# Kernel optimization log

Measured on AMD Instinct MI355X. Metric: run time of the kernel, lower is better.

Reference implementation:

```python
import jax, jax.numpy as jnp
import numpy as np

BETA = 1.0  # config.beta
B, G, K, E2 = 1024, 512, 128, 128


def setup_inputs() -> dict:
    key = jax.random.key(0)
    k1, k2, k3, k4, k5 = jax.random.split(key, 5)
    s = 0.05
    return {
        "images": jax.random.normal(k1, (B, G), dtype=jnp.float32),
        "wimg": jax.random.normal(k2, (G, K), dtype=jnp.float32) * s,    # project.weight.T
        "wrec": jax.random.normal(k3, (K, E2), dtype=jnp.float32) * s,   # rec.weight.T
        "wrec2": jax.random.normal(k4, (K + 1, E2), dtype=jnp.float32) * s,  # rec2.weight.T
        "wimg2": jax.random.normal(k5, (G, K, K + 1), dtype=jnp.float32) * s,  # img2.weight.T.reshape(K+1,K,G).T
    }


def _soft_assign(x, codes):
    # x: [B, D], codes: [D, C] -> softmax over C of -beta * mean_D (x - codes)^2
    xh = -jnp.mean((x[:, :, None] - codes[None]) ** 2, axis=1) * BETA  # [B, C]
    return jax.nn.softmax(xh, axis=-1)


def reference(images, wimg, wrec, wrec2, wimg2):
    # ---- encode ----
    xp = _soft_assign(images, wimg)            # [B, K]
    lat = xp @ wrec                            # [B, E2]
    xp = _soft_assign(lat, wrec.T)             # [B, K] (codes are wrec.T: [E2, K])
    idx = jnp.argmax(xp, axis=-1)              # [B] hard component
    xwimg = jnp.transpose(wimg2[:, idx, :], (1, 0, 2))   # [B, G, K+1]
    base = wimg[:, idx].T[:, :, None]                     # [B, G, 1]
    xd = images[:, :, None] - base - xwimg                # [B, G, K+1]
    xh2 = -jnp.mean(xd ** 2, axis=1) * BETA               # [B, K+1]
    xp2 = jax.nn.softmax(xh2, axis=-1)
    lat2 = xp2 @ wrec2                                    # [B, E2]
    # ---- decode (ret='rec', n_step>=1) ----
    xp_d = _soft_assign(lat, wrec.T)           # [B, K]
    xp2_d = _soft_assign(lat2, wrec2.T)        # [B, K+1]
    wimgg = wimg[:, :, None] + wimg2           # [G, K, K+1]
    # tensordot(xp_d[:, :, None]*xp2_d[:, None, :], wimgg.permute(1,2,0), 2)
    xrec = jnp.einsum('bk,bj,gkj->bg', xp_d, xp2_d, wimgg)  # [B, G]
    # ---- loss ----
    loss = jnp.mean((xrec - images) ** 2, axis=-1)  # [B]
    return loss
```

## Files before the change

### kernel.cpp

```cpp
#include <hip/hip_runtime.h>

#define B_    1024
#define G_    512
#define K_    128
#define J_    129
#define JP_   130
#define E2_   128
#define KK_   16512
#define KK2_  16640
#define KKE2_ 16768
#define KKP_  16896
#define SPLITS 16
#define KCHUNK 1056
#define BK_   32
#define KSTEPS 33
#define GS_   8

using short8 = __attribute__((ext_vector_type(8))) short;
using f32x4  = __attribute__((ext_vector_type(4))) float;

__device__ __forceinline__ float bf2f(unsigned short h){
  return __uint_as_float(((unsigned int)h) << 16);
}
__device__ __forceinline__ unsigned short f2bf(float f){
  unsigned int u = __float_as_uint(f);
  u += 0x7fffu + ((u >> 16) & 1u);
  return (unsigned short)(u >> 16);
}

__device__ __forceinline__ float blockSum512(float v, float* red, int t){
  #pragma unroll
  for (int off = 32; off > 0; off >>= 1) v += __shfl_down(v, off);
  __syncthreads();
  if ((t & 63) == 0) red[t >> 6] = v;
  __syncthreads();
  float r = ((red[0] + red[1]) + (red[2] + red[3]))
          + ((red[4] + red[5]) + (red[6] + red[7]));
  __syncthreads();
  return r;
}
__device__ __forceinline__ float blockMax512(float v, float* red, int t){
  #pragma unroll
  for (int off = 32; off > 0; off >>= 1) v = fmaxf(v, __shfl_down(v, off));
  __syncthreads();
  if ((t & 63) == 0) red[t >> 6] = v;
  __syncthreads();
  float r = fmaxf(fmaxf(fmaxf(red[0], red[1]), fmaxf(red[2], red[3])),
                  fmaxf(fmaxf(red[4], red[5]), fmaxf(red[6], red[7])));
  __syncthreads();
  return r;
}
__device__ __forceinline__ int blockArgmax512(float v, int i, float* redf, int* redi, int t){
  #pragma unroll
  for (int off = 32; off > 0; off >>= 1){
    float ov = __shfl_down(v, off);
    int   oi = __shfl_down(i, off);
    if (ov > v || (ov == v && oi < i)){ v = ov; i = oi; }
  }
  __syncthreads();
  if ((t & 63) == 0){ redf[t >> 6] = v; redi[t >> 6] = i; }
  __syncthreads();
  float bv = redf[0]; int bi = redi[0];
  #pragma unroll
  for (int wv = 1; wv < 8; wv++){
    float ov = redf[wv]; int oi = redi[wv];
    if (ov > bv || (ov == bv && oi < bi)){ bv = ov; bi = oi; }
  }
  __syncthreads();
  return bi;
}

__global__ __launch_bounds__(1024) void norms_kernel(
    const float* __restrict__ wimg, const float* __restrict__ wrec,
    const float* __restrict__ wrec2, float* __restrict__ c1norm,
    float* __restrict__ w3norm, float* __restrict__ w6norm,
    float* __restrict__ wrecT, float* __restrict__ wrec2T){
  int t = threadIdx.x;
  if (blockIdx.x == 0){
    __shared__ float red[8][128];
    int k = t & 127, sl = t >> 7;
    float s = 0.f;
    int g0 = sl * (G_/8);
    for (int g = g0; g < g0 + G_/8; g++){
      float v = wimg[g*K_ + k]; s += v*v;
    }
    red[sl][k] = s;
    __syncthreads();
    if (t < 128){
      float r = 0.f;
      #pragma unroll
      for (int i = 0; i < 8; i++) r += red[i][t];
      c1norm[t] = r;
    }
  } else if (blockIdx.x == 1){
    int wave = t >> 6, lane = t & 63;
    for (int k = wave; k < K_; k += 16){
      float v0 = wrec[k*E2_ + lane], v1 = wrec[k*E2_ + 64 + lane];
      float s = v0*v0 + v1*v1;
      #pragma unroll
      for (int off = 32; off > 0; off >>= 1) s += __shfl_down(s, off);
      if (lane == 0) w3norm[k] = s;
    }
  } else if (blockIdx.x == 2){
    int wave = t >> 6, lane = t & 63;
    for (int j = wave; j < J_; j += 16){
      float v0 = wrec2[j*E2_ + lane], v1 = wrec2[j*E2_ + 64 + lane];
      float s = v0*v0 + v1*v1;
      #pragma unroll
      for (int off = 32; off > 0; off >>= 1) s += __shfl_down(s, off);
      if (lane == 0) w6norm[j] = s;
    }
  } else if (blockIdx.x == 3){
    for (int n = t; n < K_*E2_; n += 1024){
      int k = n >> 7, e = n & 127;
      wrecT[e*K_ + k] = wrec[n];
    }
  } else {
    for (int n = t; n < J_*E2_; n += 1024){
      int j = n >> 7, e = n & 127;
      wrec2T[e*J_ + j] = wrec2[n];
    }
  }
}

__global__ __launch_bounds__(128) void tables_part_kernel(
    const float* __restrict__ wimg2, const float* __restrict__ wimg,
    float* __restrict__ sqp, float* __restrict__ crp,
    unsigned short* __restrict__ W2){
  int n  = blockIdx.x * 128 + threadIdx.x;
  int gs = blockIdx.y;
  int k = n / J_;
  int w2i = n + k;
  float s0=0,s1=0,s2=0,s3=0, c0=0,c1=0,c2=0,c3=0;
  int gbase = gs * (G_/GS_);
  #pragma unroll 2
  for (int g = gbase; g < gbase + G_/GS_; g += 4){
    float w0 = wimg2[(size_t)(g  )*KK_ + n];
    float w1 = wimg2[(size_t)(g+1)*KK_ + n];
    float w2 = wimg2[(size_t)(g+2)*KK_ + n];
    float w3 = wimg2[(size_t)(g+3)*KK_ + n];
    W2[(size_t)(g  )*KKP_ + w2i] = f2bf(w0);
    W2[(size_t)(g+1)*KKP_ + w2i] = f2bf(w1);
    W2[(size_t)(g+2)*KKP_ + w2i] = f2bf(w2);
    W2[(size_t)(g+3)*KKP_ + w2i] = f2bf(w3);
    s0 += w0*w0; s1 += w1*w1; s2 += w2*w2; s3 += w3*w3;
    c0 += wimg[(g  )*K_ + k]*w0;
    c1 += wimg[(g+1)*K_ + k]*w1;
    c2 += wimg[(g+2)*K_ + k]*w2;
    c3 += wimg[(g+3)*K_ + k]*w3;
  }
  sqp[(size_t)gs*KK_ + n] = (s0+s1)+(s2+s3);
  crp[(size_t)gs*KK_ + n] = (c0+c1)+(c2+c3);
}
__global__ __launch_bounds__(128) void tables_reduce_kernel(
    const float* __restrict__ sqp, const float* __restrict__ crp,
    float* __restrict__ sq2, float* __restrict__ cross){
  int n = blockIdx.x * 128 + threadIdx.x;
  float s = 0.f, c = 0.f;
  #pragma unroll
  for (int gs = 0; gs < GS_; gs++){
    s += sqp[(size_t)gs*KK_ + n];
    c += crp[(size_t)gs*KK_ + n];
  }
  sq2[n] = s; cross[n] = c;
}

__global__ __launch_bounds__(128) void w2tail_kernel(
    const float* __restrict__ wimg, unsigned short* __restrict__ W2){
  int g = blockIdx.x, t = threadIdx.x;
  unsigned short* dst = W2 + (size_t)g * KKP_;
  dst[KK2_ + t]   = f2bf(wimg[g*K_ + t]);
  dst[KKE2_ + t]  = 0;
  dst[t*JP_ + 129] = 0;
}

__global__ __launch_bounds__(512, 8) void encdec_kernel(
    const float* __restrict__ img,  const float* __restrict__ wimg,
    const float* __restrict__ wrec, const float* __restrict__ wrec2,
    const float* __restrict__ wrecT, const float* __restrict__ wrec2T,
    const unsigned short* __restrict__ W2,
    const float* __restrict__ c1norm, const float* __restrict__ w3norm,
    const float* __restrict__ w6norm, const float* __restrict__ sq2,
    const float* __restrict__ cross, unsigned short* __restrict__ Rm){
  __shared__ float simg[G_];
  __shared__ float sp[K_];
  __shared__ float sqv[J_];
  __shared__ float slat[E2_];
  __shared__ float sd1[K_];
  __shared__ float sh8[8][132];
  __shared__ float sh4[4][K_];
  __shared__ float xtra[2];
  __shared__ float redf[8];
  __shared__ int   redi[8];

  int t = threadIdx.x;
  int b = blockIdx.x;
  int tt = t & 127, q = t >> 7;
  int l = t & 63,  gs = t >> 6;

  simg[t] = img[b*G_ + t];
  __syncthreads();
  float a0 = simg[t];
  float imgnorm = blockSum512(a0*a0, redf, t);

  {
    float p0=0, p1=0;
    int g0 = gs * 64;
    const float* wbase = wimg + 2*l;
    #pragma unroll 4
    for (int g = g0; g < g0 + 64; g++){
      float2 wv = *(const float2*)(wbase + g*K_);
      float sv = simg[g];
      p0 += sv*wv.x; p1 += sv*wv.y;
    }
    sh8[gs][2*l]   = p0;
    sh8[gs][2*l+1] = p1;
  }
  __syncthreads();
  float d1 = ((sh8[0][tt] + sh8[1][tt]) + (sh8[2][tt] + sh8[3][tt]))
           + ((sh8[4][tt] + sh8[5][tt]) + (sh8[6][tt] + sh8[7][tt]));
  if (q == 0) sd1[tt] = d1;
  float xh1 = -(imgnorm - 2.f*d1 + c1norm[tt]) * (1.f/512.f);
  float m1 = blockMax512(xh1, redf, t);
  float ex1 = expf(xh1 - m1);
  float s1 = blockSum512((q == 0) ? ex1 : 0.f, redf, t);
  if (q == 0) sp[tt] = ex1 / s1;
  __syncthreads();

  {
    float l0=0,l1=0;
    int k0 = q * 32;
    for (int k = k0; k < k0 + 32; k += 2){
      l0 += sp[k  ] * wrec[(k  )*E2_ + tt];
      l1 += sp[k+1] * wrec[(k+1)*E2_ + tt];
    }
    sh4[q][tt] = l0 + l1;
  }
  __syncthreads();
  float lat = (sh4[0][tt] + sh4[1][tt]) + (sh4[2][tt] + sh4[3][tt]);
  if (q == 0) slat[tt] = lat;
  float latnorm = blockSum512((q == 0) ? lat*lat : 0.f, redf, t);

  {
    float l0=0,l1=0;
    int e0 = q * 32;
    const float* rT = wrecT + tt;
    for (int e = e0; e < e0 + 32; e += 2){
      l0 += slat[e  ] * rT[(e  )*K_];
      l1 += slat[e+1] * rT[(e+1)*K_];
    }
    sh4[q][tt] = l0 + l1;
  }
  __syncthreads();
  float d3 = (sh4[0][tt] + sh4[1][tt]) + (sh4[2][tt] + sh4[3][tt]);
  float xh3 = -(latnorm - 2.f*d3 + w3norm[tt]) * (1.f/128.f);
  float m3 = blockMax512(xh3, redf, t);
  float ex3 = expf(xh3 - m3);
  float s3 = blockSum512((q == 0) ? ex3 : 0.f, redf, t);
  if (q == 0) sp[tt] = ex3 / s3;
  int idxb = blockArgmax512(xh3, tt, redf, redi, t);
  float dsq = imgnorm - 2.f*sd1[idxb] + c1norm[idxb];

  {
    const unsigned short* Wb = W2 + (size_t)idxb * JP_ + 2*l;
    float p0=0, p1=0;
    int g0 = gs * 64;
    #pragma unroll 4
    for (int g = g0; g < g0 + 64; g++){
      unsigned int wv = *(const unsigned int*)(Wb + (size_t)g*KKP_);
      float sv = simg[g];
      p0 += sv * __uint_as_float(wv << 16);
      p1 += sv * __uint_as_float(wv & 0xffff0000u);
    }
    sh8[gs][2*l]   = p0;
    sh8[gs][2*l+1] = p1;
  }
  if (t < 64){
    const unsigned short* Wb8 = W2 + (size_t)idxb * JP_ + 128;
    float s = 0.f;
    #pragma unroll
    for (int m = 0; m < 8; m++){
      int g = t + 64*m;
      s += simg[g] * bf2f(Wb8[(size_t)g * KKP_]);
    }
    #pragma unroll
    for (int off = 32; off > 0; off >>= 1) s += __shfl_down(s, off);
    if (t == 0) xtra[0] = s;
  }
  __syncthreads();
  float xh2 = -3e38f;
  if (t < J_){
    float di = (t < 128)
      ? (((sh8[0][t] + sh8[1][t]) + (sh8[2][t] + sh8[3][t]))
       + ((sh8[4][t] + sh8[5][t]) + (sh8[6][t] + sh8[7][t])))
      : xtra[0];
    int nb = idxb*J_ + t;
    xh2 = -(dsq - 2.f*(di - cross[nb]) + sq2[nb]) * (1.f/512.f);
  }
  float m2 = blockMax512(xh2, redf, t);
  float ea = (t < J_) ? expf(xh2 - m2) : 0.f;
  float s2 = blockSum512(ea, redf, t);
  if (t < J_) sqv[t] = ea / s2;
  __syncthreads();

  {
    float lv = 0.f;
    int j0 = (q == 0) ? 0 : (q*32 + 1);
    int j1 = q*32 + 33;
    for (int j = j0; j < j1; j++)
      lv += sqv[j] * wrec2[j*E2_ + tt];
    sh4[q][tt] = lv;
  }
  __syncthreads();
  float lat2 = (sh4[0][tt] + sh4[1][tt]) + (sh4[2][tt] + sh4[3][tt]);
  if (q == 0) slat[tt] = lat2;
  float l2n = blockSum512((q == 0) ? lat2*lat2 : 0.f, redf, t);

  {
    float l0=0,l1=0;
    int e0 = q * 32;
    const float* rT = wrec2T + tt;
    for (int e = e0; e < e0 + 32; e += 2){
      l0 += slat[e  ] * rT[(e  )*J_];
      l1 += slat[e+1] * rT[(e+1)*J_];
    }
    sh4[q][tt] = l0 + l1;
  }
  if (t < 64){
    float s = slat[t]*wrec2T[t*J_ + 128] + slat[t+64]*wrec2T[(t+64)*J_ + 128];
    #pragma unroll
    for (int off = 32; off > 0; off >>= 1) s += __shfl_down(s, off);
    if (t == 0) xtra[1] = s;
  }
  __syncthreads();
  float xh6 = -3e38f;
  if (t < J_){
    float d6 = (t < 128) ? ((sh4[0][t] + sh4[1][t]) + (sh4[2][t] + sh4[3][t])) : xtra[1];
    xh6 = -(l2n - 2.f*d6 + w6norm[t]) * (1.f/128.f);
  }
  float m6 = blockMax512(xh6, redf, t);
  float e6 = (t < J_) ? expf(xh6 - m6) : 0.f;
  float s6 = blockSum512(e6, redf, t);
  if (t < J_) sqv[t] = e6 / s6;
  __syncthreads();

  unsigned short* Rrow = Rm + (size_t)b * KKP_;
  int k = t / JP_;
  int j = t - k*JP_;
  for (int kk = t; kk < KKP_; kk += 512){
    float v = 0.f;
    if (kk < KK2_){
      if (j < J_) v = sp[k] * sqv[j];
    } else if (kk < KKE2_) v = sp[kk - KK2_];
    Rrow[kk] = f2bf(v);
    j += 122;
    if (j >= JP_){ j -= JP_; k += 4; } else k += 3;
  }
}

__global__ __launch_bounds__(256) void gemm_kernel(
    const unsigned short* __restrict__ Rm, const unsigned short* __restrict__ W2,
    float* __restrict__ part){
  __shared__ __align__(16) unsigned int lds[2*128*20];
  unsigned int* lA = lds;
  unsigned int* lB = lds + 128*20;
  int tid = threadIdx.x;
  int l = tid & 63;
  int w = tid >> 6;
  int wr = (w >> 1) * 64, wc = (w & 1) * 64;
  int b0 = blockIdx.y * 128, g0 = blockIdx.x * 128;
  size_t kkbase = (size_t)blockIdx.z * KCHUNK;

  int srow = tid >> 2, scol = tid & 3;
  const unsigned short* pa = Rm + (size_t)(b0 + srow)*KKP_ + kkbase + scol*8;
  const unsigned short* pb = W2 + (size_t)(g0 + srow)*KKP_ + kkbase + scol*8;
  const size_t half = (size_t)64 * KKP_;
  unsigned int woff = srow*20 + scol*4;

  int lrow = l & 15, lko = (l >> 4) << 2;

  f32x4 zero4 = {0.f, 0.f, 0.f, 0.f};
  f32x4 acc[4][4];
  #pragma unroll
  for (int mi = 0; mi < 4; mi++)
    #pragma unroll
    for (int ni = 0; ni < 4; ni++) acc[mi][ni] = zero4;

  for (int s = 0; s < KSTEPS; s++){
    uint4 va0 = *(const uint4*)pa;
    uint4 va1 = *(const uint4*)(pa + half);
    uint4 vb0 = *(const uint4*)pb;
    uint4 vb1 = *(const uint4*)(pb + half);
    pa += BK_; pb += BK_;
    __syncthreads();
    *(uint4*)(lA + woff)          = va0;
    *(uint4*)(lA + woff + 64*20)  = va1;
    *(uint4*)(lB + woff)          = vb0;
    *(uint4*)(lB + woff + 64*20)  = vb1;
    __syncthreads();
    short8 af[4], bfv[4];
    #pragma unroll
    for (int mi = 0; mi < 4; mi++)
      af[mi] = *(const short8*)(lA + (wr + mi*16 + lrow)*20 + lko);
    #pragma unroll
    for (int ni = 0; ni < 4; ni++)
      bfv[ni] = *(const short8*)(lB + (wc + ni*16 + lrow)*20 + lko);
    #pragma unroll
    for (int mi = 0; mi < 4; mi++)
      #pragma unroll
      for (int ni = 0; ni < 4; ni++)
        acc[mi][ni] = __builtin_amdgcn_mfma_f32_16x16x32_bf16(af[mi], bfv[ni], acc[mi][ni], 0, 0, 0);
  }

  float* P = part + ((size_t)blockIdx.z * B_ + b0) * G_ + g0;
  int rh = (l >> 4) << 2, cl = l & 15;
  #pragma unroll
  for (int mi = 0; mi < 4; mi++)
    #pragma unroll
    for (int ni = 0; ni < 4; ni++)
      #pragma unroll
      for (int r = 0; r < 4; r++){
        int row = wr + mi*16 + rh + r;
        int col = wc + ni*16 + cl;
        P[(size_t)row*G_ + col] = acc[mi][ni][r];
      }
}

__global__ __launch_bounds__(128) void loss_kernel(
    const float* __restrict__ img, const float* __restrict__ part,
    float* __restrict__ out){
  __shared__ float redf[2];
  int t = threadIdx.x, b = blockIdx.x;
  float acc = 0.f;
  for (int g = t; g < G_; g += 128){
    float x = 0.f;
    #pragma unroll
    for (int z = 0; z < SPLITS; z++)
      x += part[((size_t)z*B_ + b)*G_ + g];
    float d = x - img[b*G_ + g];
    acc += d*d;
  }
  #pragma unroll
  for (int off = 32; off > 0; off >>= 1) acc += __shfl_down(acc, off);
  __syncthreads();
  if ((t & 63) == 0) redf[t >> 6] = acc;
  __syncthreads();
  if (t == 0) out[b] = (redf[0] + redf[1]) * (1.f/512.f);
}

extern "C" void kernel_launch(void* const* d_in, const int* in_sizes, int n_in,
                              void* d_out, int out_size, void* d_ws, size_t ws_size,
                              hipStream_t stream){
  (void)in_sizes; (void)n_in; (void)out_size; (void)ws_size;
  const float* img   = (const float*)d_in[0];
  const float* wimg  = (const float*)d_in[1];
  const float* wrec  = (const float*)d_in[2];
  const float* wrec2 = (const float*)d_in[3];
  const float* wimg2 = (const float*)d_in[4];
  float* out = (float*)d_out;

  char* ws = (char*)d_ws;
  size_t off = 0;
  auto alloc = [&](size_t bytes) -> void* {
    void* p = ws + off;
    off += (bytes + 255) & ~(size_t)255;
    return p;
  };
  unsigned short* W2   = (unsigned short*)alloc((size_t)G_ * KKP_ * 2);
  unsigned short* Rm   = (unsigned short*)alloc((size_t)B_ * KKP_ * 2);
  float* part   = (float*)alloc((size_t)SPLITS * B_ * G_ * 4);
  float* sqp    = (float*)alloc((size_t)GS_ * KK_ * 4);
  float* crp    = (float*)alloc((size_t)GS_ * KK_ * 4);
  float* sq2    = (float*)alloc((size_t)KK_ * 4);
  float* cross  = (float*)alloc((size_t)KK_ * 4);
  float* c1norm = (float*)alloc(K_ * 4);
  float* w3norm = (float*)alloc(K_ * 4);
  float* w6norm = (float*)alloc(J_ * 4);
  float* wrecT  = (float*)alloc((size_t)K_ * E2_ * 4);
  float* wrec2T = (float*)alloc((size_t)J_ * E2_ * 4);

  norms_kernel<<<dim3(5), dim3(1024), 0, stream>>>(wimg, wrec, wrec2, c1norm, w3norm, w6norm, wrecT, wrec2T);
  tables_part_kernel<<<dim3(129, GS_), dim3(128), 0, stream>>>(wimg2, wimg, sqp, crp, W2);
  tables_reduce_kernel<<<dim3(129), dim3(128), 0, stream>>>(sqp, crp, sq2, cross);
  w2tail_kernel<<<dim3(512), dim3(128), 0, stream>>>(wimg, W2);
  encdec_kernel<<<dim3(1024), dim3(512), 0, stream>>>(img, wimg, wrec, wrec2, wrecT, wrec2T, W2,
      c1norm, w3norm, w6norm, sq2, cross, Rm);
  gemm_kernel<<<dim3(4, 8, SPLITS), dim3(256), 0, stream>>>(Rm, W2, part);
  loss_kernel<<<dim3(1024), dim3(128), 0, stream>>>(img, part, out);
}
```

Before: 129.6 us.

## Use direct global-to-LDS loads in GEMM, fuse softmax reductions, widen vector loads

The GEMM kernel stages tiles with global_load_lds straight into LDS instead of going through registers, and drops the padded LDS row stride. To keep chunks aligned, the padded K dimension grows from 130 to 132 columns per row and KSTEPS rises to 34. The encdec kernel replaces separate max/sum/argmax block reductions with a single online max-sum(-argmax) reduction using fast exp, and widens the projection loops to float4/uint2 loads. The cost is extra padded GEMM work, possible LDS bank conflicts from the unpadded layout, and no sync between the async LDS load and its use beyond __syncthreads.

Result: faster. 126.9 us (-2.1%).

```diff
diff --git a/kernel.cpp b/kernel.cpp
--- a/kernel.cpp
+++ b/kernel.cpp
@@ -4,16 +4,16 @@
 #define G_    512
 #define K_    128
 #define J_    129
-#define JP_   130
+#define JP_   132
 #define E2_   128
 #define KK_   16512
-#define KK2_  16640
-#define KKE2_ 16768
-#define KKP_  16896
+#define KK2_  16896
+#define KKE2_ 17024
+#define KKP_  17408
 #define SPLITS 16
-#define KCHUNK 1056
+#define KCHUNK 1088
 #define BK_   32
-#define KSTEPS 33
+#define KSTEPS 34
 #define GS_   8
 
 using short8 = __attribute__((ext_vector_type(8))) short;
@@ -28,6 +28,10 @@
   return (unsigned short)(u >> 16);
 }
 
+#define GLOAD16(gptr, ldst) __builtin_amdgcn_global_load_lds( \
+    (const __attribute__((address_space(1))) unsigned int*)(gptr), \
+    (__attribute__((address_space(3))) unsigned int*)(ldst), 16, 0, 0)
+
 __device__ __forceinline__ float blockSum512(float v, float* red, int t){
   #pragma unroll
   for (int off = 32; off > 0; off >>= 1) v += __shfl_down(v, off);
@@ -39,35 +43,61 @@
   __syncthreads();
   return r;
 }
-__device__ __forceinline__ float blockMax512(float v, float* red, int t){
-  #pragma unroll
-  for (int off = 32; off > 0; off >>= 1) v = fmaxf(v, __shfl_down(v, off));
-  __syncthreads();
-  if ((t & 63) == 0) red[t >> 6] = v;
-  __syncthreads();
-  float r = fmaxf(fmaxf(fmaxf(red[0], red[1]), fmaxf(red[2], red[3])),
-                  fmaxf(fmaxf(red[4], red[5]), fmaxf(red[6], red[7])));
-  __syncthreads();
-  return r;
-}
-__device__ __forceinline__ int blockArgmax512(float v, int i, float* redf, int* redi, int t){
+
+__device__ __forceinline__ void blockSoftmaxMS512(float x, bool act,
+    float* redm, float* reds, int t, float& mo, float& so){
+  float m = x, s = act ? 1.f : 0.f;
   #pragma unroll
   for (int off = 32; off > 0; off >>= 1){
-    float ov = __shfl_down(v, off);
+    float om = __shfl_down(m, off);
+    float os = __shfl_down(s, off);
+    float nm = fmaxf(m, om);
+    s = s*__expf(m - nm) + os*__expf(om - nm);
+    m = nm;
+  }
+  __syncthreads();
+  if ((t & 63) == 0){ redm[t >> 6] = m; reds[t >> 6] = s; }
+  __syncthreads();
+  float gm = redm[0], gsv = reds[0];
+  #pragma unroll
+  for (int w = 1; w < 8; w++){
+    float om = redm[w], os = reds[w];
+    float nm = fmaxf(gm, om);
+    gsv = gsv*__expf(gm - nm) + os*__expf(om - nm);
+    gm = nm;
+  }
+  mo = gm; so = gsv;
+}
+
+__device__ __forceinline__ int blockSoftmaxMSI512(float x, int idx, bool act,
+    float* redm, float* reds, int* redi, int t, float& mo, float& so){
+  float m = x, s = act ? 1.f : 0.f; int i = idx;
+  #pragma unroll
+  for (int off = 32; off > 0; off >>= 1){
+    float om = __shfl_down(m, off);
+    float os = __shfl_down(s, off);
     int   oi = __shfl_down(i, off);
-    if (ov > v || (ov == v && oi < i)){ v = ov; i = oi; }
-  }
-  __syncthreads();
-  if ((t & 63) == 0){ redf[t >> 6] = v; redi[t >> 6] = i; }
-  __syncthreads();
-  float bv = redf[0]; int bi = redi[0];
-  #pragma unroll
-  for (int wv = 1; wv < 8; wv++){
-    float ov = redf[wv]; int oi = redi[wv];
-    if (ov > bv || (ov == bv && oi < bi)){ bv = ov; bi = oi; }
-  }
-  __syncthreads();
-  return bi;
+    bool take = (om > m) || (om == m && oi < i);
+    float nm = fmaxf(m, om);
+    s = s*__expf(m - nm) + os*__expf(om - nm);
+    i = take ? oi : i;
+    m = nm;
+  }
+  __syncthreads();
+  if ((t & 63) == 0){ redm[t >> 6] = m; reds[t >> 6] = s; redi[t >> 6] = i; }
+  __syncthreads();
+  float gm = redm[0], gsv = reds[0]; int gi = redi[0];
+  #pragma unroll
+  for (int w = 1; w < 8; w++){
+    float om = redm[w], os = reds[w]; int oi = redi[w];
+    bool take = (om > gm) || (om == gm && oi < gi);
+    float nm = fmaxf(gm, om);
+    gsv = gsv*__expf(gm - nm) + os*__expf(om - nm);
+    gi = take ? oi : gi;
+    gm = nm;
+  }
+  mo = gm; so = gsv;
+  return gi;
 }
 
 __global__ __launch_bounds__(1024) void norms_kernel(
@@ -130,7 +160,7 @@
   int n  = blockIdx.x * 128 + threadIdx.x;
   int gs = blockIdx.y;
   int k = n / J_;
-  int w2i = n + k;
+  int w2i = n + 3*k;
   float s0=0,s1=0,s2=0,s3=0, c0=0,c1=0,c2=0,c3=0;
   int gbase = gs * (G_/GS_);
   #pragma unroll 2
@@ -169,9 +199,13 @@
     const float* __restrict__ wimg, unsigned short* __restrict__ W2){
   int g = blockIdx.x, t = threadIdx.x;
   unsigned short* dst = W2 + (size_t)g * KKP_;
-  dst[KK2_ + t]   = f2bf(wimg[g*K_ + t]);
-  dst[KKE2_ + t]  = 0;
+  dst[KK2_ + t]        = f2bf(wimg[g*K_ + t]);
+  dst[KKE2_ + t]       = 0;
+  dst[KKE2_ + 128 + t] = 0;
+  dst[KKE2_ + 256 + t] = 0;
   dst[t*JP_ + 129] = 0;
+  dst[t*JP_ + 130] = 0;
+  dst[t*JP_ + 131] = 0;
 }
 
 __global__ __launch_bounds__(512, 8) void encdec_kernel(
@@ -182,49 +216,50 @@
     const float* __restrict__ c1norm, const float* __restrict__ w3norm,
     const float* __restrict__ w6norm, const float* __restrict__ sq2,
     const float* __restrict__ cross, unsigned short* __restrict__ Rm){
-  __shared__ float simg[G_];
+  __shared__ __align__(16) float simg[G_];
   __shared__ float sp[K_];
   __shared__ float sqv[J_];
   __shared__ float slat[E2_];
   __shared__ float sd1[K_];
-  __shared__ float sh8[8][132];
+  __shared__ __align__(16) float sh16[16][128];
   __shared__ float sh4[4][K_];
   __shared__ float xtra[2];
-  __shared__ float redf[8];
+  __shared__ float redm[8], reds[8];
   __shared__ int   redi[8];
 
   int t = threadIdx.x;
   int b = blockIdx.x;
   int tt = t & 127, q = t >> 7;
-  int l = t & 63,  gs = t >> 6;
+  int ll = t & 31, gq = t >> 5;
 
   simg[t] = img[b*G_ + t];
   __syncthreads();
   float a0 = simg[t];
-  float imgnorm = blockSum512(a0*a0, redf, t);
+  float imgnorm = blockSum512(a0*a0, redm, t);
 
   {
-    float p0=0, p1=0;
-    int g0 = gs * 64;
-    const float* wbase = wimg + 2*l;
+    float p0=0,p1=0,p2=0,p3=0;
+    int g0 = gq * 32;
     #pragma unroll 4
-    for (int g = g0; g < g0 + 64; g++){
-      float2 wv = *(const float2*)(wbase + g*K_);
+    for (int g = g0; g < g0 + 32; g++){
+      float4 wv = *(const float4*)(wimg + g*K_ + 4*ll);
       float sv = simg[g];
-      p0 += sv*wv.x; p1 += sv*wv.y;
-    }
-    sh8[gs][2*l]   = p0;
-    sh8[gs][2*l+1] = p1;
-  }
-  __syncthreads();
-  float d1 = ((sh8[0][tt] + sh8[1][tt]) + (sh8[2][tt] + sh8[3][tt]))
-           + ((sh8[4][tt] + sh8[5][tt]) + (sh8[6][tt] + sh8[7][tt]));
-  if (q == 0) sd1[tt] = d1;
-  float xh1 = -(imgnorm - 2.f*d1 + c1norm[tt]) * (1.f/512.f);
-  float m1 = blockMax512(xh1, redf, t);
-  float ex1 = expf(xh1 - m1);
-  float s1 = blockSum512((q == 0) ? ex1 : 0.f, redf, t);
-  if (q == 0) sp[tt] = ex1 / s1;
+      p0 += sv*wv.x; p1 += sv*wv.y; p2 += sv*wv.z; p3 += sv*wv.w;
+    }
+    float4 st = {p0, p1, p2, p3};
+    *(float4*)&sh16[gq][4*ll] = st;
+  }
+  __syncthreads();
+  float xh1 = -3e38f, d1 = 0.f;
+  if (t < 128){
+    #pragma unroll
+    for (int i = 0; i < 16; i++) d1 += sh16[i][t];
+    sd1[t] = d1;
+    xh1 = -(imgnorm - 2.f*d1 + c1norm[t]) * (1.f/512.f);
+  }
+  float m1, s1;
+  blockSoftmaxMS512(xh1, t < 128, redm, reds, t, m1, s1);
+  if (t < 128) sp[t] = __expf(xh1 - m1) / s1;
   __syncthreads();
 
   {
@@ -239,7 +274,7 @@
   __syncthreads();
   float lat = (sh4[0][tt] + sh4[1][tt]) + (sh4[2][tt] + sh4[3][tt]);
   if (q == 0) slat[tt] = lat;
-  float latnorm = blockSum512((q == 0) ? lat*lat : 0.f, redf, t);
+  float latnorm = blockSum512((q == 0) ? lat*lat : 0.f, redm, t);
 
   {
     float l0=0,l1=0;
@@ -252,28 +287,31 @@
     sh4[q][tt] = l0 + l1;
   }
   __syncthreads();
-  float d3 = (sh4[0][tt] + sh4[1][tt]) + (sh4[2][tt] + sh4[3][tt]);
-  float xh3 = -(latnorm - 2.f*d3 + w3norm[tt]) * (1.f/128.f);
-  float m3 = blockMax512(xh3, redf, t);
-  float ex3 = expf(xh3 - m3);
-  float s3 = blockSum512((q == 0) ? ex3 : 0.f, redf, t);
-  if (q == 0) sp[tt] = ex3 / s3;
-  int idxb = blockArgmax512(xh3, tt, redf, redi, t);
+  float xh3 = -3e38f;
+  if (t < 128){
+    float d3 = (sh4[0][t] + sh4[1][t]) + (sh4[2][t] + sh4[3][t]);
+    xh3 = -(latnorm - 2.f*d3 + w3norm[t]) * (1.f/128.f);
+  }
+  float m3, s3;
+  int idxb = blockSoftmaxMSI512(xh3, tt, t < 128, redm, reds, redi, t, m3, s3);
+  if (t < 128) sp[t] = __expf(xh3 - m3) / s3;
   float dsq = imgnorm - 2.f*sd1[idxb] + c1norm[idxb];
 
   {
-    const unsigned short* Wb = W2 + (size_t)idxb * JP_ + 2*l;
-    float p0=0, p1=0;
-    int g0 = gs * 64;
+    const unsigned short* Wb = W2 + (size_t)idxb * JP_ + 4*ll;
+    float p0=0,p1=0,p2=0,p3=0;
+    int g0 = gq * 32;
     #pragma unroll 4
-    for (int g = g0; g < g0 + 64; g++){
-      unsigned int wv = *(const unsigned int*)(Wb + (size_t)g*KKP_);
+    for (int g = g0; g < g0 + 32; g++){
+      uint2 wv = *(const uint2*)(Wb + (size_t)g*KKP_);
       float sv = simg[g];
-      p0 += sv * __uint_as_float(wv << 16);
-      p1 += sv * __uint_as_float(wv & 0xffff0000u);
-    }
-    sh8[gs][2*l]   = p0;
-    sh8[gs][2*l+1] = p1;
+      p0 += sv * __uint_as_float(wv.x << 16);
+      p1 += sv * __uint_as_float(wv.x & 0xffff0000u);
+      p2 += sv * __uint_as_float(wv.y << 16);
+      p3 += sv * __uint_as_float(wv.y & 0xffff0000u);
+    }
+    float4 st = {p0, p1, p2, p3};
+    *(float4*)&sh16[gq][4*ll] = st;
   }
   if (t < 64){
     const unsigned short* Wb8 = W2 + (size_t)idxb * JP_ + 128;
@@ -290,17 +328,18 @@
   __syncthreads();
   float xh2 = -3e38f;
   if (t < J_){
-    float di = (t < 128)
-      ? (((sh8[0][t] + sh8[1][t]) + (sh8[2][t] + sh8[3][t]))
-       + ((sh8[4][t] + sh8[5][t]) + (sh8[6][t] + sh8[7][t])))
-      : xtra[0];
+    float di;
+    if (t < 128){
+      di = 0.f;
+      #pragma unroll
+      for (int i = 0; i < 16; i++) di += sh16[i][t];
+    } else di = xtra[0];
     int nb = idxb*J_ + t;
     xh2 = -(dsq - 2.f*(di - cross[nb]) + sq2[nb]) * (1.f/512.f);
   }
-  float m2 = blockMax512(xh2, redf, t);
-  float ea = (t < J_) ? expf(xh2 - m2) : 0.f;
-  float s2 = blockSum512(ea, redf, t);
-  if (t < J_) sqv[t] = ea / s2;
+  float m2, s2;
+  blockSoftmaxMS512(xh2, t < J_, redm, reds, t, m2, s2);
+  if (t < J_) sqv[t] = __expf(xh2 - m2) / s2;
   __syncthreads();
 
   {
@@ -314,7 +353,7 @@
   __syncthreads();
   float lat2 = (sh4[0][tt] + sh4[1][tt]) + (sh4[2][tt] + sh4[3][tt]);
   if (q == 0) slat[tt] = lat2;
-  float l2n = blockSum512((q == 0) ? lat2*lat2 : 0.f, redf, t);
+  float l2n = blockSum512((q == 0) ? lat2*lat2 : 0.f, redm, t);
 
   {
     float l0=0,l1=0;
@@ -338,10 +377,9 @@
     float d6 = (t < 128) ? ((sh4[0][t] + sh4[1][t]) + (sh4[2][t] + sh4[3][t])) : xtra[1];
     xh6 = -(l2n - 2.f*d6 + w6norm[t]) * (1.f/128.f);
   }
-  float m6 = blockMax512(xh6, redf, t);
-  float e6 = (t < J_) ? expf(xh6 - m6) : 0.f;
-  float s6 = blockSum512(e6, redf, t);
-  if (t < J_) sqv[t] = e6 / s6;
+  float m6, s6;
+  blockSoftmaxMS512(xh6, t < J_, redm, reds, t, m6, s6);
+  if (t < J_) sqv[t] = __expf(xh6 - m6) / s6;
   __syncthreads();
 
   unsigned short* Rrow = Rm + (size_t)b * KKP_;
@@ -353,7 +391,7 @@
       if (j < J_) v = sp[k] * sqv[j];
     } else if (kk < KKE2_) v = sp[kk - KK2_];
     Rrow[kk] = f2bf(v);
-    j += 122;
+    j += 116;
     if (j >= JP_){ j -= JP_; k += 4; } else k += 3;
   }
 }
@@ -361,21 +399,23 @@
 __global__ __launch_bounds__(256) void gemm_kernel(
     const unsigned short* __restrict__ Rm, const unsigned short* __restrict__ W2,
     float* __restrict__ part){
-  __shared__ __align__(16) unsigned int lds[2*128*20];
+  __shared__ __align__(16) unsigned int lds[4096];
   unsigned int* lA = lds;
-  unsigned int* lB = lds + 128*20;
+  unsigned int* lB = lds + 2048;
+  auto lA3 = (__attribute__((address_space(3))) unsigned int*)lA;
+  auto lB3 = (__attribute__((address_space(3))) unsigned int*)lB;
   int tid = threadIdx.x;
   int l = tid & 63;
-  int w = tid >> 6;
-  int wr = (w >> 1) * 64, wc = (w & 1) * 64;
+  int wv = tid >> 6;
+  int wr = (wv >> 1) * 64, wc = (wv & 1) * 64;
   int b0 = blockIdx.y * 128, g0 = blockIdx.x * 128;
   size_t kkbase = (size_t)blockIdx.z * KCHUNK;
 
   int srow = tid >> 2, scol = tid & 3;
-  const unsigned short* pa = Rm + (size_t)(b0 + srow)*KKP_ + kkbase + scol*8;
-  const unsigned short* pb = W2 + (size_t)(g0 + srow)*KKP_ + kkbase + scol*8;
-  const size_t half = (size_t)64 * KKP_;
-  unsigned int woff = srow*20 + scol*4;
+  const unsigned short* ga  = Rm + (size_t)(b0 + srow)*KKP_ + kkbase + scol*8;
+  const unsigned short* ga2 = ga + (size_t)64 * KKP_;
+  const unsigned short* gb  = W2 + (size_t)(g0 + srow)*KKP_ + kkbase + scol*8;
+  const unsigned short* gb2 = gb + (size_t)64 * KKP_;
 
   int lrow = l & 15, lko = (l >> 4) << 2;
 
@@ -387,24 +427,20 @@
     for (int ni = 0; ni < 4; ni++) acc[mi][ni] = zero4;
 
   for (int s = 0; s < KSTEPS; s++){
-    uint4 va0 = *(const uint4*)pa;
-    uint4 va1 = *(const uint4*)(pa + half);
-    uint4 vb0 = *(const uint4*)pb;
-    uint4 vb1 = *(const uint4*)(pb + half);
-    pa += BK_; pb += BK_;
     __syncthreads();
-    *(uint4*)(lA + woff)          = va0;
-    *(uint4*)(lA + woff + 64*20)  = va1;
-    *(uint4*)(lB + woff)          = vb0;
-    *(uint4*)(lB + woff + 64*20)  = vb1;
+    GLOAD16(ga,  lA3 + wv*256);
+    GLOAD16(ga2, lA3 + 1024 + wv*256);
+    GLOAD16(gb,  lB3 + wv*256);
+    GLOAD16(gb2, lB3 + 1024 + wv*256);
+    ga += BK_; ga2 += BK_; gb += BK_; gb2 += BK_;
     __syncthreads();
     short8 af[4], bfv[4];
     #pragma unroll
     for (int mi = 0; mi < 4; mi++)
-      af[mi] = *(const short8*)(lA + (wr + mi*16 + lrow)*20 + lko);
+      af[mi] = *(const short8*)(lA + (wr + mi*16 + lrow)*16 + lko);
     #pragma unroll
     for (int ni = 0; ni < 4; ni++)
-      bfv[ni] = *(const short8*)(lB + (wc + ni*16 + lrow)*20 + lko);
+      bfv[ni] = *(const short8*)(lB + (wc + ni*16 + lrow)*16 + lko);
     #pragma unroll
     for (int mi = 0; mi < 4; mi++)
       #pragma unroll
```
